# Kernel tuning notes

Measured on AMD Instinct MI355X. Metric: run time of the kernel, lower is better.

## Reference

```python
import jax, jax.numpy as jnp
import numpy as np


def setup_inputs() -> dict:
    key = jax.random.key(0)
    k1, k2 = jax.random.split(key)
    B, C, H, W = 16, 32, 32, 32
    NUM = 32
    x = jax.random.normal(k1, (B, C, H, W), dtype=jnp.float32)
    # torch init: (rand(num, depth, 9) - 0.5) * 1
    neighbors = jax.random.uniform(k2, (NUM, C, 9), dtype=jnp.float32) - 0.5
    return {"x": x, "neighbors": neighbors}


def reference(x, neighbors):
    """ConvNearestNeightbor forward.

    For each of the 9 zero-padded 3x3 shifts of x, compute |x_shift - neighbor|
    broadcast over the `num` codebook axis, and take the elementwise max over
    the 9 shifts. Equivalent to the torch code's max over dim=3 of the
    (B, num, C, 9, H, W) abs-diff tensor, but computed incrementally so the
    9-axis intermediate is never materialized.
    """
    B, C, H, W = x.shape
    num = neighbors.shape[0]
    xp = jnp.pad(x, ((0, 0), (0, 0), (1, 1), (1, 1)))  # zero borders
    out = None
    k = 0
    for row in (-1, 0, 1):
        for col in (-1, 0, 1):
            # y[b,c,k,i,j] = x[b,c,i-row,j-col] (0 outside) == padded slice
            xs = xp[:, :, 1 - row:1 - row + H, 1 - col:1 - col + W]  # (B,C,H,W)
            nb = neighbors[:, :, k]                                  # (num,C)
            d = jnp.abs(xs[:, None] - nb[None, :, :, None, None])    # (B,num,C,H,W)
            out = d if out is None else jnp.maximum(out, d)
            k += 1
    return out.reshape(B, num * C, H, W)
```

## Files before the change

kernel.cpp:

```cpp
#include <hip/hip_runtime.h>


#define BB 16
#define CC 32
#define HH 32
#define WW 32
#define NUMN 32
#define NPB 4

typedef float f32x4 __attribute__((ext_vector_type(4)));

__global__ __launch_bounds__(256) void conv_nn_kernel(
    const float* __restrict__ x,
    const float* __restrict__ neighbors,
    float* __restrict__ out)
{
    __shared__ float tile[HH + 2][WW + 4];
    __shared__ float nlds[NPB * 9];

    const int bc = blockIdx.x;
    const int b  = bc >> 5;
    const int c  = bc & 31;
    const int n0 = blockIdx.y * NPB;
    const int t  = threadIdx.x;

    const float* xplane = x + (b * CC + c) * (HH * WW);
    for (int idx = t; idx < 34 * 34; idx += 256) {
        int row = idx / 34;
        int col = idx - row * 34;
        int h = row - 1, w = col - 1;
        float v = 0.0f;
        if ((unsigned)h < (unsigned)HH && (unsigned)w < (unsigned)WW)
            v = xplane[h * WW + w];
        tile[row][col] = v;
    }
    if (t < NPB * 9) {
        int n = t / 9;
        int k = t - n * 9;
        nlds[t] = neighbors[((n0 + n) * CC + c) * 9 + k];
    }
    __syncthreads();

    const int h  = t >> 3;
    const int w0 = (t & 7) * 4;

    float xr[3][6];
    #pragma unroll
    for (int r = 0; r < 3; ++r)
        #pragma unroll
        for (int j = 0; j < 6; ++j)
            xr[r][j] = tile[h + r][w0 + j];

    float* oplane = out + (size_t)((b * NUMN + n0) * CC + c) * (HH * WW) + t * 4;
    const int nstride = CC * HH * WW;

    #pragma unroll
    for (int ni = 0; ni < NPB; ++ni) {
        float nb[9];
        #pragma unroll
        for (int k = 0; k < 9; ++k) nb[k] = nlds[ni * 9 + k];

        float acc0 = fabsf(xr[2][2] - nb[0]);
        float acc1 = fabsf(xr[2][3] - nb[0]);
        float acc2 = fabsf(xr[2][4] - nb[0]);
        float acc3 = fabsf(xr[2][5] - nb[0]);
        #pragma unroll
        for (int kk = 1; kk < 9; ++kk) {
            const int rr  = kk / 3;
            const int cc2 = kk - rr * 3;
            const float nv = nb[kk];
            acc0 = fmaxf(acc0, fabsf(xr[2 - rr][0 + 2 - cc2] - nv));
            acc1 = fmaxf(acc1, fabsf(xr[2 - rr][1 + 2 - cc2] - nv));
            acc2 = fmaxf(acc2, fabsf(xr[2 - rr][2 + 2 - cc2] - nv));
            acc3 = fmaxf(acc3, fabsf(xr[2 - rr][3 + 2 - cc2] - nv));
        }
        f32x4 v = { acc0, acc1, acc2, acc3 };
        __builtin_nontemporal_store(v,
            reinterpret_cast<f32x4*>(oplane + (size_t)ni * nstride));
    }
}

extern "C" void kernel_launch(void* const* d_in, const int* in_sizes, int n_in,
                              void* d_out, int out_size, void* d_ws, size_t ws_size,
                              hipStream_t stream) {
    const float* x         = (const float*)d_in[0];
    const float* neighbors = (const float*)d_in[1];
    float* out             = (float*)d_out;

    dim3 grid(BB * CC, NUMN / NPB);
    dim3 block(256);
    conv_nn_kernel<<<grid, block, 0, stream>>>(x, neighbors, out);
}
```

Before: 85.52 us.

## Remap blocks to (b,n) with channel loop, load x directly without LDS

Each block now handles one (batch, neighbor) pair and loops over 8 channels, instead of one (batch, channel) plane across 4 neighbors. The input halo is read straight from global memory with vector loads and bounds predicates, so the LDS tile and the barrier go away. Each block also writes 8 contiguous output planes. The output store changes from nontemporal to a normal store. The cost is that every input plane is now re-read from global memory/L2 by 32 blocks instead of being staged once, and neighbor values are read with scalar global loads.

```diff
diff --git a/kernel.cpp b/kernel.cpp
--- a/kernel.cpp
+++ b/kernel.cpp
@@ -6,7 +6,7 @@
 #define HH 32
 #define WW 32
 #define NUMN 32
-#define NPB 4
+#define CPB 8
 
 typedef float f32x4 __attribute__((ext_vector_type(4)));
 
@@ -15,50 +15,51 @@
     const float* __restrict__ neighbors,
     float* __restrict__ out)
 {
-    __shared__ float tile[HH + 2][WW + 4];
-    __shared__ float nlds[NPB * 9];
-
-    const int bc = blockIdx.x;
-    const int b  = bc >> 5;
-    const int c  = bc & 31;
-    const int n0 = blockIdx.y * NPB;
+    const int bn = blockIdx.x;
+    const int b  = bn >> 5;
+    const int n  = bn & 31;
+    const int c0 = blockIdx.y * CPB;
     const int t  = threadIdx.x;
-
-    const float* xplane = x + (b * CC + c) * (HH * WW);
-    for (int idx = t; idx < 34 * 34; idx += 256) {
-        int row = idx / 34;
-        int col = idx - row * 34;
-        int h = row - 1, w = col - 1;
-        float v = 0.0f;
-        if ((unsigned)h < (unsigned)HH && (unsigned)w < (unsigned)WW)
-            v = xplane[h * WW + w];
-        tile[row][col] = v;
-    }
-    if (t < NPB * 9) {
-        int n = t / 9;
-        int k = t - n * 9;
-        nlds[t] = neighbors[((n0 + n) * CC + c) * 9 + k];
-    }
-    __syncthreads();
 
     const int h  = t >> 3;
     const int w0 = (t & 7) * 4;
 
-    float xr[3][6];
-    #pragma unroll
-    for (int r = 0; r < 3; ++r)
-        #pragma unroll
-        for (int j = 0; j < 6; ++j)
-            xr[r][j] = tile[h + r][w0 + j];
+    const int row0 = h - 1, row2 = h + 1;
+    const bool rv0 = (row0 >= 0);
+    const bool rv2 = (row2 < HH);
+    const bool lv  = (w0 > 0);
+    const bool rgt = (w0 + 4 < WW);
 
-    float* oplane = out + (size_t)((b * NUMN + n0) * CC + c) * (HH * WW) + t * 4;
-    const int nstride = CC * HH * WW;
+    float* obase = out + ((size_t)(b * NUMN + n) * CC + c0) * (HH * WW) + t * 4;
 
-    #pragma unroll
-    for (int ni = 0; ni < NPB; ++ni) {
+    #pragma unroll 2
+    for (int ci = 0; ci < CPB; ++ci) {
+        const int c = c0 + ci;
+        const float* __restrict__ rp1 = x + (b * CC + c) * (HH * WW) + h * WW;
+
+        float xr[3][6];
+        {
+            const float* rp0 = rp1 - WW;
+            const float* rp2 = rp1 + WW;
+            f32x4 m0 = {0,0,0,0}, m1, m2 = {0,0,0,0};
+            if (rv0) m0 = *reinterpret_cast<const f32x4*>(rp0 + w0);
+            m1 = *reinterpret_cast<const f32x4*>(rp1 + w0);
+            if (rv2) m2 = *reinterpret_cast<const f32x4*>(rp2 + w0);
+            xr[0][0] = (rv0 && lv)  ? rp0[w0 - 1] : 0.0f;
+            xr[0][5] = (rv0 && rgt) ? rp0[w0 + 4] : 0.0f;
+            xr[1][0] = lv  ? rp1[w0 - 1] : 0.0f;
+            xr[1][5] = rgt ? rp1[w0 + 4] : 0.0f;
+            xr[2][0] = (rv2 && lv)  ? rp2[w0 - 1] : 0.0f;
+            xr[2][5] = (rv2 && rgt) ? rp2[w0 + 4] : 0.0f;
+            xr[0][1] = m0.x; xr[0][2] = m0.y; xr[0][3] = m0.z; xr[0][4] = m0.w;
+            xr[1][1] = m1.x; xr[1][2] = m1.y; xr[1][3] = m1.z; xr[1][4] = m1.w;
+            xr[2][1] = m2.x; xr[2][2] = m2.y; xr[2][3] = m2.z; xr[2][4] = m2.w;
+        }
+
         float nb[9];
         #pragma unroll
-        for (int k = 0; k < 9; ++k) nb[k] = nlds[ni * 9 + k];
+        for (int k = 0; k < 9; ++k)
+            nb[k] = neighbors[(n * CC + c) * 9 + k];
 
         float acc0 = fabsf(xr[2][2] - nb[0]);
         float acc1 = fabsf(xr[2][3] - nb[0]);
@@ -75,8 +76,7 @@
             acc3 = fmaxf(acc3, fabsf(xr[2 - rr][3 + 2 - cc2] - nv));
         }
         f32x4 v = { acc0, acc1, acc2, acc3 };
-        __builtin_nontemporal_store(v,
-            reinterpret_cast<f32x4*>(oplane + (size_t)ni * nstride));
+        *reinterpret_cast<f32x4*>(obase + ci * (HH * WW)) = v;
     }
 }
 
@@ -87,7 +87,7 @@
     const float* neighbors = (const float*)d_in[1];
     float* out             = (float*)d_out;
 
-    dim3 grid(BB * CC, NUMN / NPB);
+    dim3 grid(BB * NUMN, CC / CPB);
     dim3 block(256);
     conv_nn_kernel<<<grid, block, 0, stream>>>(x, neighbors, out);
 }
```

Result: slower. 99.41 us (+16.2%).
